# Kernel optimization log

Hardware: AMD Instinct MI355X
Metric: run time of the kernel (lower is better)

## Reference

```python
import jax, jax.numpy as jnp
import numpy as np

C_S = 1024
C_Z = 128
H = 16
D = C_S // H  # 64
INF = 1000000.0
B, I, J = 1, 1024, 1024


def setup_inputs() -> dict:
    key = jax.random.key(0)
    ks = jax.random.split(key, 10)
    sc = 0.02
    return {
        "s": jax.random.normal(ks[0], (B, I, C_S), jnp.float32),
        "k_in": jax.random.normal(ks[1], (B, J, C_S), jnp.float32),
        "mask": jnp.ones((B, J), jnp.float32),
        "bias": jax.random.normal(ks[2], (B, I, J, C_Z), jnp.float32),
        "Wq": jax.random.normal(ks[3], (C_S, C_S), jnp.float32) * sc,
        "bq": jax.random.normal(ks[4], (C_S,), jnp.float32) * sc,
        "Wk": jax.random.normal(ks[5], (C_S, C_S), jnp.float32) * sc,
        "Wv": jax.random.normal(ks[6], (C_S, C_S), jnp.float32) * sc,
        "Wg": jax.random.normal(ks[7], (C_S, C_S), jnp.float32) * sc,
        "Wo": jax.random.normal(ks[8], (C_S, C_S), jnp.float32) * sc,
        "Wz": jax.random.normal(ks[9], (C_Z, H), jnp.float32) * sc,
        "multiplicity": 1,
    }


def reference(s, k_in, mask, bias, Wq, bq, Wk, Wv, Wg, Wo, Wz, multiplicity):
    b = s.shape[0]
    # QKV projections (torch Linear: x @ W.T + b)
    q = (s @ Wq.T + bq).reshape(b, -1, H, D)        # [b, i, h, d]
    k = (k_in @ Wk.T).reshape(b, -1, H, D)          # [b, j, h, d]
    v = (k_in @ Wv.T).reshape(b, -1, H, D)          # [b, j, h, d]

    # pair bias: proj_z = Linear(c_z -> h, no bias) + rearrange to [b, h, i, j]
    z = jnp.einsum("bijc,ch->bhij", bias, Wz)
    z = jnp.repeat(z, multiplicity, axis=0)
    z = z + (1.0 - mask[:, None, None, :]) * (-INF)  # mask over key dim j

    g = jax.nn.sigmoid(s @ Wg.T)                    # [b, i, c_s]

    # attention in fp32 (original uses autocast-disabled fp32 block)
    attn = jnp.einsum("bihd,bjhd->bhij", q.astype(jnp.float32), k.astype(jnp.float32))
    attn = attn / (D ** 0.5) + z.astype(jnp.float32)
    attn = jax.nn.softmax(attn, axis=-1)
    o = jnp.einsum("bhij,bjhd->bihd", attn, v.astype(jnp.float32)).astype(v.dtype)

    o = o.reshape(b, -1, C_S)
    return (g * o) @ Wo.T
```

## Files before the change

### kernel.cpp

```cpp
#include <hip/hip_runtime.h>

typedef unsigned short u16;
typedef unsigned int   u32;
typedef __attribute__((ext_vector_type(8))) short bf16x8;
typedef __attribute__((ext_vector_type(4))) float f32x4;

#define MFMA16(a, b, c) __builtin_amdgcn_mfma_f32_16x16x32_bf16((a), (b), (c), 0, 0, 0)

__device__ __forceinline__ float bfu(u16 x) { return __uint_as_float(((u32)x) << 16); }
__device__ __forceinline__ u16 f2bf(float f) {
    u32 u = __float_as_uint(f);
    u32 r = u + 0x7fffu + ((u >> 16) & 1u);
    return (u16)(r >> 16);
}
__device__ __forceinline__ u32 pk2(float a, float b) {
    return (u32)f2bf(a) | ((u32)f2bf(b) << 16);
}
__device__ __forceinline__ bf16x8 cvt8(float4 a, float4 b) {
    bf16x8 r;
    r[0] = (short)f2bf(a.x); r[1] = (short)f2bf(a.y);
    r[2] = (short)f2bf(a.z); r[3] = (short)f2bf(a.w);
    r[4] = (short)f2bf(b.x); r[5] = (short)f2bf(b.y);
    r[6] = (short)f2bf(b.z); r[7] = (short)f2bf(b.w);
    return r;
}
__device__ __forceinline__ void gl_lds16(const u16* g, u16* l) {
    __builtin_amdgcn_global_load_lds(
        (const __attribute__((address_space(1))) void*)g,
        (__attribute__((address_space(3))) void*)l, 16, 0, 0);
}

struct CvtArgs { const float* src[7]; u16* dst[7]; };

__global__ __launch_bounds__(256) void zproj_cvt(
    const float* __restrict__ bias, const float* __restrict__ Wz,
    u16* __restrict__ z, CvtArgs ca)
{
    __shared__ float lz[16 * 516];
    const int t = threadIdx.x;

    if (blockIdx.x >= 2048) {
        const int blk  = blockIdx.x - 2048;
        const int tsel = blk >> 6;
        const float* s = ca.src[tsel];
        u16* d = ca.dst[tsel];
        const int base = (blk & 63) * 16384;
        #pragma unroll 4
        for (int it = 0; it < 16; ++it) {
            const int idx = base + (it * 256 + t) * 4;
            float4 v = *(const float4*)(s + idx);
            uint2 p;
            p.x = pk2(v.x, v.y);
            p.y = pk2(v.z, v.w);
            *(uint2*)(d + idx) = p;
        }
        return;
    }

    const int lane = t & 63, w = t >> 6;
    const int ln = lane & 15, q4 = lane >> 4;
    const int row0 = blockIdx.x * 512;

    bf16x8 bfrag[4];
    #pragma unroll
    for (int kb = 0; kb < 4; ++kb)
        #pragma unroll
        for (int j = 0; j < 8; ++j)
            bfrag[kb][j] = (short)f2bf(Wz[(kb * 32 + q4 * 8 + j) * 16 + ln]);

    #pragma unroll 1
    for (int it = 0; it < 8; ++it) {
        const int rloc = (it * 4 + w) * 16;
        const float* ap = bias + (size_t)(row0 + rloc + ln) * 128 + q4 * 8;
        f32x4 c = {0, 0, 0, 0};
        #pragma unroll
        for (int kb = 0; kb < 4; ++kb) {
            float4 x0 = *(const float4*)(ap + kb * 32);
            float4 x1 = *(const float4*)(ap + kb * 32 + 4);
            bf16x8 a = cvt8(x0, x1);
            c = MFMA16(a, bfrag[kb], c);
        }
        #pragma unroll
        for (int r = 0; r < 4; ++r)
            lz[ln * 516 + rloc + q4 * 4 + r] = c[r];
    }
    __syncthreads();
    #pragma unroll 4
    for (int rep = 0; rep < 32; ++rep) {
        const int idx = rep * 256 + t;
        const int hh = idx >> 9, r = idx & 511;
        z[(size_t)hh * 1048576 + row0 + r] = f2bf(lz[hh * 516 + r]);
    }
}

__global__ __launch_bounds__(256) void gemm_qkvg(
    const u16* __restrict__ sb, const u16* __restrict__ kbf,
    const u16* __restrict__ Wqb, const u16* __restrict__ Wgb,
    const u16* __restrict__ Wkb, const u16* __restrict__ Wvb,
    const float* __restrict__ bqv,
    u16* __restrict__ q, u16* __restrict__ g,
    u16* __restrict__ kk, u16* __restrict__ vT)
{
    __shared__ u16 lA[64 * 64];
    __shared__ u16 lB[64 * 64];
    const int zb = blockIdx.z;
    const u16* Ab = zb ? kbf : sb;
    const u16* W0 = zb ? Wkb : Wqb;
    const u16* W1 = zb ? Wvb : Wgb;

    const int t = threadIdx.x, lane = t & 63, w = t >> 6;
    const int ln = lane & 15, q4 = lane >> 4;
    const int wm = (w & 1) * 32, wn = (w >> 1) * 32;
    const int m0 = blockIdx.y * 64, n0 = blockIdx.x * 64;

    const u16* Wp = (n0 < 1024) ? (W0 + (size_t)n0 * 1024)
                                : (W1 + (size_t)(n0 - 1024) * 1024);
    const int srow = t >> 3, scol = (t & 7) * 8;
    const u16* ga = Ab + (m0 + srow) * 1024 + scol;
    const u16* gb = Wp + srow * 1024 + scol;
    u16* la = lA + t * 8;
    u16* lb = lB + t * 8;

    f32x4 acc00 = {0,0,0,0}, acc01 = {0,0,0,0}, acc10 = {0,0,0,0}, acc11 = {0,0,0,0};

    for (int k0 = 0; k0 < 1024; k0 += 64) {
        gl_lds16(ga + k0,             la);
        gl_lds16(ga + k0 + 32 * 1024, la + 32 * 64);
        gl_lds16(gb + k0,             lb);
        gl_lds16(gb + k0 + 32 * 1024, lb + 32 * 64);
        __syncthreads();
        #pragma unroll
        for (int ks = 0; ks < 2; ++ks) {
            bf16x8 a0 = *(const bf16x8*)(lA + (wm +      ln) * 64 + ks * 32 + q4 * 8);
            bf16x8 a1 = *(const bf16x8*)(lA + (wm + 16 + ln) * 64 + ks * 32 + q4 * 8);
            bf16x8 b0 = *(const bf16x8*)(lB + (wn +      ln) * 64 + ks * 32 + q4 * 8);
            bf16x8 b1 = *(const bf16x8*)(lB + (wn + 16 + ln) * 64 + ks * 32 + q4 * 8);
            acc00 = MFMA16(a0, b0, acc00);
            acc01 = MFMA16(a0, b1, acc01);
            acc10 = MFMA16(a1, b0, acc10);
            acc11 = MFMA16(a1, b1, acc11);
        }
        __syncthreads();
    }

    #pragma unroll
    for (int tm = 0; tm < 2; ++tm) {
        #pragma unroll
        for (int tn = 0; tn < 2; ++tn) {
            const f32x4 a = (tm == 0) ? (tn == 0 ? acc00 : acc01)
                                      : (tn == 0 ? acc10 : acc11);
            #pragma unroll
            for (int r = 0; r < 4; ++r) {
                const int gm = m0 + wm + tm * 16 + q4 * 4 + r;
                const int gn = n0 + wn + tn * 16 + ln;
                float cv = a[r];
                if (zb == 0) {
                    if (gn < 1024) q[gm * 1024 + gn] = f2bf(cv + bqv[gn]);
                    else g[gm * 1024 + gn - 1024] = f2bf(1.0f / (1.0f + __expf(-cv)));
                } else {
                    if (gn < 1024) kk[gm * 1024 + gn] = f2bf(cv);
                    else vT[(gn - 1024) * 1024 + gm] = f2bf(cv);
                }
            }
        }
    }
}

__global__ __launch_bounds__(256) void attn_kernel(
    const u16* __restrict__ qb, const u16* __restrict__ kmat,
    const u16* __restrict__ vT, const u16* __restrict__ zb,
    const float* __restrict__ maskb, const u16* __restrict__ gmat,
    u16* __restrict__ o)
{
    __shared__ u16 pbf[16 * 1032];
    __shared__ float redm[4][16];
    __shared__ float reds[4][16];
    const int h = blockIdx.y;
    const int i0 = blockIdx.x * 16;
    const int t = threadIdx.x, lane = t & 63, w = t >> 6;
    const int ln = lane & 15, q4 = lane >> 4;

    const u16* qp = qb + (i0 + ln) * 1024 + h * 64 + q4 * 8;
    const bf16x8 aq0 = *(const bf16x8*)(qp);
    const bf16x8 aq1 = *(const bf16x8*)(qp + 32);

    f32x4 s[16];
    #pragma unroll
    for (int u = 0; u < 16; ++u) {
        const int j0 = (w * 16 + u) * 16;
        const u16* kp = kmat + (j0 + ln) * 1024 + h * 64 + q4 * 8;
        bf16x8 b0 = *(const bf16x8*)(kp);
        bf16x8 b1 = *(const bf16x8*)(kp + 32);
        f32x4 c = {0, 0, 0, 0};
        c = MFMA16(aq0, b0, c);
        c = MFMA16(aq1, b1, c);
        const int j = j0 + ln;
        const float mt = (1.0f - maskb[j]) * (-1000000.0f);
        #pragma unroll
        for (int r = 0; r < 4; ++r) {
            const int gi = i0 + q4 * 4 + r;
            c[r] = c[r] * 0.125f + bfu(zb[(size_t)h * 1048576 + gi * 1024 + j]) + mt;
        }
        s[u] = c;
    }

    float mx[4];
    #pragma unroll
    for (int r = 0; r < 4; ++r) {
        float m_ = s[0][r];
        #pragma unroll
        for (int u = 1; u < 16; ++u) m_ = fmaxf(m_, s[u][r]);
        #pragma unroll
        for (int off = 1; off < 16; off <<= 1) m_ = fmaxf(m_, __shfl_xor(m_, off));
        mx[r] = m_;
    }
    if (ln == 0) {
        #pragma unroll
        for (int r = 0; r < 4; ++r) redm[w][q4 * 4 + r] = mx[r];
    }
    __syncthreads();

    float inv[4];
    #pragma unroll
    for (int r = 0; r < 4; ++r) {
        const int row = q4 * 4 + r;
        const float m_ = fmaxf(fmaxf(redm[0][row], redm[1][row]),
                               fmaxf(redm[2][row], redm[3][row]));
        float s_ = 0.f;
        #pragma unroll
        for (int u = 0; u < 16; ++u) {
            float e = __expf(s[u][r] - m_);
            s[u][r] = e;
            s_ += e;
        }
        #pragma unroll
        for (int off = 1; off < 16; off <<= 1) s_ += __shfl_xor(s_, off);
        mx[r] = s_;
    }
    if (ln == 0) {
        #pragma unroll
        for (int r = 0; r < 4; ++r) reds[w][q4 * 4 + r] = mx[r];
    }
    __syncthreads();
    #pragma unroll
    for (int r = 0; r < 4; ++r) {
        const int row = q4 * 4 + r;
        inv[r] = 1.0f / (reds[0][row] + reds[1][row] + reds[2][row] + reds[3][row]);
    }

    #pragma unroll
    for (int u = 0; u < 16; ++u) {
        const int j0 = (w * 16 + u) * 16;
        #pragma unroll
        for (int r = 0; r < 4; ++r)
            pbf[(q4 * 4 + r) * 1032 + j0 + ln] = f2bf(s[u][r] * inv[r]);
    }
    __syncthreads();

    f32x4 oc = {0, 0, 0, 0};
    #pragma unroll 4
    for (int ks = 0; ks < 32; ++ks) {
        bf16x8 pa = *(const bf16x8*)(pbf + ln * 1032 + ks * 32 + q4 * 8);
        bf16x8 vb = *(const bf16x8*)(vT + (h * 64 + w * 16 + ln) * 1024 + ks * 32 + q4 * 8);
        oc = MFMA16(pa, vb, oc);
    }
    const int col = h * 64 + w * 16 + ln;
    #pragma unroll
    for (int r = 0; r < 4; ++r) {
        const int gi = i0 + q4 * 4 + r;
        const float gv = bfu(gmat[gi * 1024 + col]);
        o[gi * 1024 + col] = f2bf(oc[r] * gv);
    }
}

__global__ __launch_bounds__(256) void gemm_out_sk(
    const u16* __restrict__ og, const u16* __restrict__ Wob, float* __restrict__ pbuf)
{
    __shared__ u16 lA[64 * 64];
    __shared__ u16 lB[64 * 64];
    const int t = threadIdx.x, lane = t & 63, w = t >> 6;
    const int ln = lane & 15, q4 = lane >> 4;
    const int wm = (w & 1) * 32, wn = (w >> 1) * 32;
    const int m0 = blockIdx.y * 64, n0 = blockIdx.x * 64;
    const int kz = blockIdx.z;

    const int srow = t >> 3, scol = (t & 7) * 8;
    const u16* ga = og  + (m0 + srow) * 1024 + scol + kz * 256;
    const u16* gb = Wob + (n0 + srow) * 1024 + scol + kz * 256;
    u16* la = lA + t * 8;
    u16* lb = lB + t * 8;

    f32x4 acc00 = {0,0,0,0}, acc01 = {0,0,0,0}, acc10 = {0,0,0,0}, acc11 = {0,0,0,0};

    for (int k0 = 0; k0 < 256; k0 += 64) {
        gl_lds16(ga + k0,             la);
        gl_lds16(ga + k0 + 32 * 1024, la + 32 * 64);
        gl_lds16(gb + k0,             lb);
        gl_lds16(gb + k0 + 32 * 1024, lb + 32 * 64);
        __syncthreads();
        #pragma unroll
        for (int ks = 0; ks < 2; ++ks) {
            bf16x8 a0 = *(const bf16x8*)(lA + (wm +      ln) * 64 + ks * 32 + q4 * 8);
            bf16x8 a1 = *(const bf16x8*)(lA + (wm + 16 + ln) * 64 + ks * 32 + q4 * 8);
            bf16x8 b0 = *(const bf16x8*)(lB + (wn +      ln) * 64 + ks * 32 + q4 * 8);
            bf16x8 b1 = *(const bf16x8*)(lB + (wn + 16 + ln) * 64 + ks * 32 + q4 * 8);
            acc00 = MFMA16(a0, b0, acc00);
            acc01 = MFMA16(a0, b1, acc01);
            acc10 = MFMA16(a1, b0, acc10);
            acc11 = MFMA16(a1, b1, acc11);
        }
        __syncthreads();
    }

    float* pz = pbuf + (size_t)kz * 1048576;
    #pragma unroll
    for (int tm = 0; tm < 2; ++tm) {
        #pragma unroll
        for (int tn = 0; tn < 2; ++tn) {
            const f32x4 a = (tm == 0) ? (tn == 0 ? acc00 : acc01)
                                      : (tn == 0 ? acc10 : acc11);
            #pragma unroll
            for (int r = 0; r < 4; ++r) {
                const int gm = m0 + wm + tm * 16 + q4 * 4 + r;
                const int gn = n0 + wn + tn * 16 + ln;
                pz[gm * 1024 + gn] = a[r];
            }
        }
    }
}

__global__ __launch_bounds__(256) void reduce4(
    const float* __restrict__ p, float* __restrict__ out)
{
    const int idx = (blockIdx.x * 256 + threadIdx.x) * 4;
    float4 a = *(const float4*)(p + idx);
    float4 b = *(const float4*)(p + 1048576 + idx);
    float4 c = *(const float4*)(p + 2097152 + idx);
    float4 d = *(const float4*)(p + 3145728 + idx);
    float4 r;
    r.x = (a.x + b.x) + (c.x + d.x);
    r.y = (a.y + b.y) + (c.y + d.y);
    r.z = (a.z + b.z) + (c.z + d.z);
    r.w = (a.w + b.w) + (c.w + d.w);
    *(float4*)(out + idx) = r;
}

extern "C" void kernel_launch(void* const* d_in, const int* in_sizes, int n_in,
                              void* d_out, int out_size, void* d_ws, size_t ws_size,
                              hipStream_t stream)
{
    const float* s_in = (const float*)d_in[0];
    const float* k_in = (const float*)d_in[1];
    const float* mask = (const float*)d_in[2];
    const float* bias = (const float*)d_in[3];
    const float* Wq   = (const float*)d_in[4];
    const float* bq   = (const float*)d_in[5];
    const float* Wk   = (const float*)d_in[6];
    const float* Wv   = (const float*)d_in[7];
    const float* Wg   = (const float*)d_in[8];
    const float* Wo   = (const float*)d_in[9];
    const float* Wz   = (const float*)d_in[10];

    char* ws = (char*)d_ws;
    const size_t MB = 1 << 20;
    u16* sb  = (u16*)(ws + 0 * MB);
    u16* kbf = (u16*)(ws + 2 * MB);
    u16* Wqb = (u16*)(ws + 4 * MB);
    u16* Wkb = (u16*)(ws + 6 * MB);
    u16* Wvb = (u16*)(ws + 8 * MB);
    u16* Wgb = (u16*)(ws + 10 * MB);
    u16* Wob = (u16*)(ws + 12 * MB);
    u16* q   = (u16*)(ws + 14 * MB);
    u16* kk  = (u16*)(ws + 16 * MB);
    u16* vT  = (u16*)(ws + 18 * MB);
    u16* g   = (u16*)(ws + 20 * MB);
    u16* og  = (u16*)(ws + 22 * MB);
    u16* z   = (u16*)(ws + 24 * MB);
    float* pbuf = (float*)(ws + 56 * MB);
    float* out = (float*)d_out;

    CvtArgs ca;
    ca.src[0] = s_in; ca.dst[0] = sb;
    ca.src[1] = k_in; ca.dst[1] = kbf;
    ca.src[2] = Wq;   ca.dst[2] = Wqb;
    ca.src[3] = Wk;   ca.dst[3] = Wkb;
    ca.src[4] = Wv;   ca.dst[4] = Wvb;
    ca.src[5] = Wg;   ca.dst[5] = Wgb;
    ca.src[6] = Wo;   ca.dst[6] = Wob;

    const dim3 blk(256);
    hipLaunchKernelGGL(zproj_cvt, dim3(2496), blk, 0, stream, bias, Wz, z, ca);
    hipLaunchKernelGGL(gemm_qkvg, dim3(32, 16, 2), blk, 0, stream,
                       sb, kbf, Wqb, Wgb, Wkb, Wvb, bq, q, g, kk, vT);
    hipLaunchKernelGGL(attn_kernel, dim3(64, 16), blk, 0, stream,
                       q, kk, vT, z, mask, g, og);
    hipLaunchKernelGGL(gemm_out_sk, dim3(16, 16, 4), blk, 0, stream, og, Wob, pbuf);
    hipLaunchKernelGGL(reduce4, dim3(1024), blk, 0, stream, pbuf, out);
}
```

Before: 801.3 us.

## Stage bias and z tiles through LDS via async global_load_lds with swizzle

The z-projection kernel now streams bias rows into LDS with global_load_lds in 64-row chunks, using an XOR swizzle to avoid bank conflicts, and writes z through a bf16 LDS buffer with 16-byte vector stores. The attention kernel prefetches its 16x1024 z tile into LDS asynchronously while loading Q, then reads bias values from swizzled LDS instead of scattered 2-byte global loads. It also reuses the same LDS buffer for the P matrix. The aim is coalesced, wide global traffic, at the cost of extra barriers and larger shared memory, which may reduce occupancy.

```diff
diff --git a/kernel.cpp b/kernel.cpp
--- a/kernel.cpp
+++ b/kernel.cpp
@@ -24,7 +24,7 @@
     r[6] = (short)f2bf(b.z); r[7] = (short)f2bf(b.w);
     return r;
 }
-__device__ __forceinline__ void gl_lds16(const u16* g, u16* l) {
+__device__ __forceinline__ void gl_lds16(const void* g, void* l) {
     __builtin_amdgcn_global_load_lds(
         (const __attribute__((address_space(1))) void*)g,
         (__attribute__((address_space(3))) void*)l, 16, 0, 0);
@@ -36,7 +36,7 @@
     const float* __restrict__ bias, const float* __restrict__ Wz,
     u16* __restrict__ z, CvtArgs ca)
 {
-    __shared__ float lz[16 * 516];
+    __shared__ __align__(16) char smem[64 * 512];
     const int t = threadIdx.x;
 
     if (blockIdx.x >= 2048) {
@@ -60,6 +60,7 @@
     const int lane = t & 63, w = t >> 6;
     const int ln = lane & 15, q4 = lane >> 4;
     const int row0 = blockIdx.x * 512;
+    const int sxor = (ln & 7) << 4;
 
     bf16x8 bfrag[4];
     #pragma unroll
@@ -68,28 +69,47 @@
         for (int j = 0; j < 8; ++j)
             bfrag[kb][j] = (short)f2bf(Wz[(kb * 32 + q4 * 8 + j) * 16 + ln]);
 
-    #pragma unroll 1
-    for (int it = 0; it < 8; ++it) {
-        const int rloc = (it * 4 + w) * 16;
-        const float* ap = bias + (size_t)(row0 + rloc + ln) * 128 + q4 * 8;
-        f32x4 c = {0, 0, 0, 0};
+    f32x4 c[8];
+    const char* gb = (const char*)(bias + (size_t)row0 * 128);
+    const int rbase = (w * 16 + ln) * 512;
+
+    #pragma unroll
+    for (int ch = 0; ch < 8; ++ch) {
+        const char* gsrc = gb + ch * (64 * 512);
+        #pragma unroll
+        for (int cc = 0; cc < 8; ++cc) {
+            const int o   = (w * 8 + cc) * 1024 + lane * 16;
+            const int src = o ^ (((o >> 9) & 7) << 4);
+            gl_lds16(gsrc + src, smem + (w * 8 + cc) * 1024);
+        }
+        __syncthreads();
+        f32x4 acc = {0, 0, 0, 0};
         #pragma unroll
         for (int kb = 0; kb < 4; ++kb) {
-            float4 x0 = *(const float4*)(ap + kb * 32);
-            float4 x1 = *(const float4*)(ap + kb * 32 + 4);
-            bf16x8 a = cvt8(x0, x1);
-            c = MFMA16(a, bfrag[kb], c);
-        }
+            const int p = rbase + kb * 128 + q4 * 32;
+            float4 x0 = *(const float4*)(smem + ((p     ) ^ sxor));
+            float4 x1 = *(const float4*)(smem + ((p + 16) ^ sxor));
+            acc = MFMA16(cvt8(x0, x1), bfrag[kb], acc);
+        }
+        c[ch] = acc;
+        __syncthreads();
+    }
+
+    u16* zbuf = (u16*)smem;
+    #pragma unroll
+    for (int ch = 0; ch < 8; ++ch)
         #pragma unroll
         for (int r = 0; r < 4; ++r)
-            lz[ln * 516 + rloc + q4 * 4 + r] = c[r];
-    }
+            zbuf[ln * 520 + ch * 64 + w * 16 + q4 * 4 + r] = f2bf(c[ch][r]);
     __syncthreads();
-    #pragma unroll 4
-    for (int rep = 0; rep < 32; ++rep) {
-        const int idx = rep * 256 + t;
-        const int hh = idx >> 9, r = idx & 511;
-        z[(size_t)hh * 1048576 + row0 + r] = f2bf(lz[hh * 516 + r]);
+
+    {
+        const int hh = t >> 4, c0 = (t & 15) * 32;
+        u16* zg = z + (size_t)hh * 1048576 + row0 + c0;
+        const u16* zs = zbuf + hh * 520 + c0;
+        #pragma unroll
+        for (int n = 0; n < 4; ++n)
+            *(uint4*)(zg + n * 8) = *(const uint4*)(zs + n * 8);
     }
 }
 
@@ -172,7 +192,7 @@
     const float* __restrict__ maskb, const u16* __restrict__ gmat,
     u16* __restrict__ o)
 {
-    __shared__ u16 pbf[16 * 1032];
+    __shared__ __align__(16) char smem[16 * 1032 * 2];
     __shared__ float redm[4][16];
     __shared__ float reds[4][16];
     const int h = blockIdx.y;
@@ -180,9 +200,21 @@
     const int t = threadIdx.x, lane = t & 63, w = t >> 6;
     const int ln = lane & 15, q4 = lane >> 4;
 
+    {
+        const char* zsl = (const char*)(zb + (size_t)h * 1048576 + (size_t)i0 * 1024);
+        #pragma unroll
+        for (int cc = 0; cc < 8; ++cc) {
+            const int o_  = (w * 8 + cc) * 1024 + lane * 16;
+            const int src = (o_ & ~2047) + ((o_ & 2047) ^ (((o_ >> 11) & 7) << 4));
+            gl_lds16(zsl + src, smem + (w * 8 + cc) * 1024);
+        }
+    }
+
     const u16* qp = qb + (i0 + ln) * 1024 + h * 64 + q4 * 8;
     const bf16x8 aq0 = *(const bf16x8*)(qp);
     const bf16x8 aq1 = *(const bf16x8*)(qp + 32);
+
+    __syncthreads();
 
     f32x4 s[16];
     #pragma unroll
@@ -196,10 +228,12 @@
         c = MFMA16(aq1, b1, c);
         const int j = j0 + ln;
         const float mt = (1.0f - maskb[j]) * (-1000000.0f);
+        const int cb = (j0 + ln) * 2;
         #pragma unroll
         for (int r = 0; r < 4; ++r) {
-            const int gi = i0 + q4 * 4 + r;
-            c[r] = c[r] * 0.125f + bfu(zb[(size_t)h * 1048576 + gi * 1024 + j]) + mt;
+            const int row = q4 * 4 + r;
+            const u16 zv = *(const u16*)(smem + row * 2048 + (cb ^ ((row & 7) << 4)));
+            c[r] = c[r] * 0.125f + bfu(zv) + mt;
         }
         s[u] = c;
     }
@@ -248,6 +282,7 @@
         inv[r] = 1.0f / (reds[0][row] + reds[1][row] + reds[2][row] + reds[3][row]);
     }
 
+    u16* pbf = (u16*)smem;
     #pragma unroll
     for (int u = 0; u < 16; ++u) {
         const int j0 = (w * 16 + u) * 16;
```

After: 793.1 us. No clear change (-1.0%).
